# Kernel optimization log

Measured on AMD Instinct MI355X. Metric: run time of the kernel, lower is better.

Reference implementation:

```python
import jax, jax.numpy as jnp
import numpy as np

C, D, K15, K16, OUT = 64, 8, 15, 16, 512
B = 32768


def setup_inputs() -> dict:
    key = jax.random.key(0)
    kx, kS, kH, kT, kL = jax.random.split(key, 5)
    x = jax.random.normal(kx, (B, C * D), dtype=jnp.float32)
    S = jax.random.normal(kS, (C, D, K15), dtype=jnp.float32)
    H = jax.random.normal(kH, (K15, K16), dtype=jnp.float32)
    T = jax.random.normal(kT, (C, K15), dtype=jnp.float32)
    LUT = jax.random.normal(kL, (C, K16, OUT), dtype=jnp.float32)
    return {"x": x, "S": S, "H": H, "T": T, "LUT": LUT}


def reference(x, S, H, T, LUT):
    b = x.shape[0]
    xv = x.reshape(b, C, D)                              # (B, C, D)
    p = jnp.einsum('bcd,cdk->bck', xv, S) - T            # (B, C, 15)
    # torch sets zeros to -1 before sign => sign(x)==-1 when x<=0
    s = jnp.where(p > 0, jnp.float32(1.0), jnp.float32(-1.0))
    h = jnp.einsum('bck,kj->bcj', s, H)                  # (B, C, 16)
    idx = jnp.argmax(h, axis=-1)                         # (B, C) int
    # one_hot @ LUT == direct gather of LUT[c, idx[b,c], :]
    vals = LUT[jnp.arange(C)[None, :], idx]              # (B, C, OUT)
    return jnp.sum(vals, axis=1)                         # (B, OUT)
```

## Files before the change

kernel.cpp:

```cpp
#include <hip/hip_runtime.h>
#include <stdint.h>

#define B_    32768
#define C_    64
#define D_    8
#define K15_  15
#define K16_  16
#define OUT_  512

typedef _Float16 half4v __attribute__((ext_vector_type(4)));
typedef _Float16 half8  __attribute__((ext_vector_type(8)));
typedef uint32_t uint4v __attribute__((ext_vector_type(4)));

#define AMAP_OFF  0
#define AMAP_SZ   32768
#define S64_OFF   32768
#define S64_SZ    (64 * 15 * 8 * 8)
#define T64_OFF   (S64_OFF + S64_SZ)
#define T64_SZ    (64 * 15 * 8)
#define IDX_OFF   (T64_OFF + T64_SZ)
#define IDX_SZ    (B_ * C_)
#define S32_SZ    (64 * 15 * 8 * 4)
#define PCT_OFF   (IDX_OFF + IDX_SZ)
#define PCT_SZ    (B_ * 32)
#define PTAB_OFF  (PCT_OFF + PCT_SZ)
#define PTAB_SZ   (32 * 32 * 256 * 16 * 2)
#define WS_NEED   ((size_t)PTAB_OFF + PTAB_SZ)

__device__ __forceinline__ void gld_lds16(const void* g, void* l) {
    __builtin_amdgcn_global_load_lds(
        (const __attribute__((address_space(1))) void*)g,
        (__attribute__((address_space(3))) void*)l, 16, 0, 0);
}

__device__ __forceinline__ void fma_mix_lo(float& acc, uint32_t w, float one) {
    asm("v_fma_mix_f32 %0, %1, %2, %0 op_sel_hi:[1,0,0]"
        : "+v"(acc) : "v"(w), "v"(one));
}
__device__ __forceinline__ void fma_mix_hi(float& acc, uint32_t w, float one) {
    asm("v_fma_mix_f32 %0, %1, %2, %0 op_sel:[1,0,0] op_sel_hi:[1,0,0]"
        : "+v"(acc) : "v"(w), "v"(one));
}

__global__ __launch_bounds__(256) void k_setup(const float* __restrict__ LUT,
                                               const float* __restrict__ H,
                                               const float* __restrict__ S,
                                               const float* __restrict__ T,
                                               _Float16* __restrict__ P5,
                                               uint8_t* __restrict__ amap,
                                               double* __restrict__ S64,
                                               double* __restrict__ T64,
                                               float* __restrict__ S32,
                                               float* __restrict__ T32,
                                               int do_pairs) {
    int gid = blockIdx.x * 256 + threadIdx.x;

    if (do_pairs) {
        int e8 = gid & 1;
        int q = (gid >> 1) & 255;
        int jc = (gid >> 9) & 31;
        int p = gid >> 14;
        int t0 = q >> 4;
        int t1 = q & 15;
        int j0 = jc * 16 + e8 * 8;
        const float* u = LUT + (size_t)((2 * p) * 16 + t0) * 512 + j0;
        const float* v = LUT + (size_t)((2 * p + 1) * 16 + t1) * 512 + j0;
        float4 u0 = ((const float4*)u)[0];
        float4 u1 = ((const float4*)u)[1];
        float4 v0 = ((const float4*)v)[0];
        float4 v1 = ((const float4*)v)[1];
        half8 w;
        w[0] = (_Float16)(u0.x + v0.x);
        w[1] = (_Float16)(u0.y + v0.y);
        w[2] = (_Float16)(u0.z + v0.z);
        w[3] = (_Float16)(u0.w + v0.w);
        w[4] = (_Float16)(u1.x + v1.x);
        w[5] = (_Float16)(u1.y + v1.y);
        w[6] = (_Float16)(u1.z + v1.z);
        w[7] = (_Float16)(u1.w + v1.w);
        *(half8*)(P5 + (size_t)gid * 8) = w;
    }

    if (blockIdx.x < 128) {
        int code = gid;
        double h[K16_];
#pragma unroll
        for (int j = 0; j < K16_; ++j) h[j] = 0.0;
#pragma unroll
        for (int k = 0; k < K15_; ++k) {
            double s = ((code >> k) & 1) ? 1.0 : -1.0;
#pragma unroll
            for (int j = 0; j < K16_; ++j) h[j] += s * (double)H[k * K16_ + j];
        }
        double best = h[0];
        int bi = 0;
#pragma unroll
        for (int j = 1; j < K16_; ++j) {
            if (h[j] > best) { best = h[j]; bi = j; }
        }
        amap[code] = (uint8_t)bi;
    } else if (blockIdx.x == 128) {
        for (int i = threadIdx.x; i < 64 * 15 * 8; i += 256) {
            int c = i / 120;
            int r = i - c * 120;
            int k = r >> 3;
            int d = r & 7;
            float sv = S[c * 120 + d * 15 + k];
            S64[i] = (double)sv;
            if (do_pairs) S32[i] = sv;
        }
        for (int i = threadIdx.x; i < 64 * 15; i += 256) {
            T64[i] = (double)T[i];
            if (do_pairs) T32[i] = T[i];
        }
    }
}

#define XST3 579
#define CPAD2 24
template <int FAST>
__global__ __launch_bounds__(256, 6) void k_codes5(const float* __restrict__ x,
                                                   const double* __restrict__ S64,
                                                   const double* __restrict__ T64,
                                                   const float* __restrict__ S32,
                                                   const float* __restrict__ T32,
                                                   const uint8_t* __restrict__ amap,
                                                   uint8_t* __restrict__ idxo,
                                                   uint8_t* __restrict__ pcT) {
    __shared__ float xls[8 * XST3];
    __shared__ alignas(16) uint16_t codesh[64 * CPAD2];

    int bg = blockIdx.x >> 2;
    int cq = blockIdx.x & 3;
    int b0 = bg * 64;
    int lane = threadIdx.x & 63;
    int wv = __builtin_amdgcn_readfirstlane(threadIdx.x >> 6);
    int tid = threadIdx.x;

    float4 rgA[4], rgB[4];
#pragma unroll
    for (int t2 = 0; t2 < 4; ++t2) {
        int e = t2 * 256 + tid;
        int b = e >> 4;
        int j4 = e & 15;
        rgA[t2] = *(const float4*)(x + (size_t)(b0 + b) * 512 + cq * 128 +
                                   0 * 64 + j4 * 4);
    }
#pragma unroll
    for (int t2 = 0; t2 < 4; ++t2) {
        int e = t2 * 256 + tid;
        int b = e >> 4;
        int j4 = e & 15;
        int cl = j4 >> 1;
        int d0 = (j4 & 1) * 4;
        float* dst = &xls[cl * XST3 + b * 9 + d0];
        dst[0] = rgA[t2].x; dst[1] = rgA[t2].y;
        dst[2] = rgA[t2].z; dst[3] = rgA[t2].w;
    }
    __syncthreads();

#pragma unroll
    for (int t2 = 0; t2 < 4; ++t2) {
        int e = t2 * 256 + tid;
        int b = e >> 4;
        int j4 = e & 15;
        rgB[t2] = *(const float4*)(x + (size_t)(b0 + b) * 512 + cq * 128 +
                                   1 * 64 + j4 * 4);
    }

#pragma unroll
    for (int r = 0; r < 2; ++r) {
#pragma unroll
        for (int i = 0; i < 2; ++i) {
            int cl = wv + i * 4;
            int c = cq * 16 + r * 8 + cl;
            unsigned code = 0;
            if (FAST) {
                const float* Sc = S32 + c * 120;
                const float* Tc = T32 + c * 15;
                float xf[8];
#pragma unroll
                for (int d = 0; d < 8; ++d)
                    xf[d] = xls[cl * XST3 + lane * 9 + d];
                float pmin = 3.0e38f;
#pragma unroll
                for (int k = 0; k < K15_; ++k) {
                    float p = -Tc[k];
#pragma unroll
                    for (int d = 0; d < 8; ++d)
                        p = fmaf(xf[d], Sc[k * 8 + d], p);
                    code |= (p > 0.f) ? (1u << k) : 0u;
                    pmin = fminf(pmin, fabsf(p));
                }
                if (pmin < 1e-4f) {
                    const double* Sd = S64 + c * 120;
                    const double* Td = T64 + c * 15;
                    code = 0;
#pragma unroll
                    for (int k = 0; k < K15_; ++k) {
                        double p = -Td[k];
#pragma unroll
                        for (int d = 0; d < 8; ++d)
                            p = fma((double)xf[d], Sd[k * 8 + d], p);
                        code |= (p > 0.0) ? (1u << k) : 0u;
                    }
                }
            } else {
                const double* Sc = S64 + c * 120;
                const double* Tc = T64 + c * 15;
                double xd[8];
#pragma unroll
                for (int d = 0; d < 8; ++d)
                    xd[d] = (double)xls[cl * XST3 + lane * 9 + d];
#pragma unroll
                for (int k = 0; k < K15_; ++k) {
                    double p = -Tc[k];
#pragma unroll
                    for (int d = 0; d < 8; ++d)
                        p = fma(xd[d], Sc[k * 8 + d], p);
                    code |= (p > 0.0) ? (1u << k) : 0u;
                }
            }
            codesh[lane * CPAD2 + r * 8 + cl] = (uint16_t)code;
        }
        if (r == 0) {
            __syncthreads();
#pragma unroll
            for (int t2 = 0; t2 < 4; ++t2) {
                int e = t2 * 256 + tid;
                int b = e >> 4;
                int j4 = e & 15;
                int cl = j4 >> 1;
                int d0 = (j4 & 1) * 4;
                float* dst = &xls[cl * XST3 + b * 9 + d0];
                dst[0] = rgB[t2].x; dst[1] = rgB[t2].y;
                dst[2] = rgB[t2].z; dst[3] = rgB[t2].w;
            }
            __syncthreads();
        }
    }
    __syncthreads();

    int bb = tid >> 2;
    int sub = tid & 3;
    uint64_t cw8 = *(const uint64_t*)&codesh[bb * CPAD2 + sub * 4];
    uint16_t cds[4];
    cds[0] = (uint16_t)(cw8 & 0xFFFF);
    cds[1] = (uint16_t)((cw8 >> 16) & 0xFFFF);
    cds[2] = (uint16_t)((cw8 >> 32) & 0xFFFF);
    cds[3] = (uint16_t)(cw8 >> 48);
    uint8_t ids[4];
#pragma unroll
    for (int j = 0; j < 4; ++j) ids[j] = amap[cds[j]];

    if (FAST) {
        int row = b0 + bb;
        int rg = row >> 10;
        int tr = row & 127;
        int i_ = (row & 1023) >> 7;
        uint8_t* base = pcT + rg * 1024 + tr * 8 + i_;
        int p0 = cq * 8 + sub * 2;
        base[(size_t)p0 * 32768] = (uint8_t)((ids[0] << 4) | ids[1]);
        base[(size_t)(p0 + 1) * 32768] = (uint8_t)((ids[2] << 4) | ids[3]);
    } else {
        uint32_t w0 = (uint32_t)ids[0] | ((uint32_t)ids[1] << 8) |
                      ((uint32_t)ids[2] << 16) | ((uint32_t)ids[3] << 24);
        *(uint32_t*)(idxo + (size_t)(b0 + bb) * 64 + cq * 16 + sub * 4) = w0;
    }
}

__global__ __launch_bounds__(256, 8) void k_main9(const uint8_t* __restrict__ pcT,
                                                  const _Float16* __restrict__ P5,
                                                  float* __restrict__ out) {
    __shared__ alignas(16) _Float16 slab[2][256 * 16];

    int rg5 = blockIdx.x >> 5;
    int jc = blockIdx.x & 31;
    int t = threadIdx.x;
    int tc = t & 1;
    int tr = t >> 1;
    int lane = t & 63;
    int wv = __builtin_amdgcn_readfirstlane(t >> 6);

    const uint8_t* cbase = pcT + (rg5 >> 1) * 1024 + tr * 8 + (rg5 & 1) * 4;

    float acc[4][8];
#pragma unroll
    for (int i = 0; i < 4; ++i)
#pragma unroll
        for (int e = 0; e < 8; ++e) acc[i][e] = 0.f;
    float one = 1.0f;

    int hoff = wv * 512 + lane * 8;

    {
        const _Float16* g = P5 + (size_t)jc * 4096 + hoff;
        gld_lds16(g, &slab[0][wv * 512]);
        gld_lds16(g + 2048, &slab[0][wv * 512 + 2048]);
    }
    uint32_t cw = *(const uint32_t*)cbase;
    uint32_t cwn = 0;

    for (int p = 0; p < 32; ++p) {
        __syncthreads();

        if (p < 31) {
            const _Float16* g =
                P5 + (size_t)((p + 1) * 32 + jc) * 4096 + hoff;
            _Float16* d = &slab[(p + 1) & 1][wv * 512];
            gld_lds16(g, d);
            gld_lds16(g + 2048, d + 2048);
            cwn = *(const uint32_t*)(cbase + (size_t)(p + 1) * 32768);
        }

        const _Float16* rb = &slab[p & 1][0] + tc * 8;
        uint32_t cw_cur = cw;
#pragma unroll
        for (int i = 0; i < 4; ++i) {
            int ci = (int)((cw_cur >> (8 * i)) & 0xFF);
            half8 v = *(const half8*)(rb + ci * 16);
            uint4v w = __builtin_bit_cast(uint4v, v);
#pragma unroll
            for (int e2 = 0; e2 < 4; ++e2) {
                fma_mix_lo(acc[i][2 * e2], w[e2], one);
                fma_mix_hi(acc[i][2 * e2 + 1], w[e2], one);
            }
        }
        cw = cwn;
    }

#pragma unroll
    for (int i = 0; i < 4; ++i) {
        int row = rg5 * 512 + i * 128 + tr;
        float* o = out + (size_t)row * 512 + jc * 16 + tc * 8;
        float4 w0;
        w0.x = acc[i][0]; w0.y = acc[i][1]; w0.z = acc[i][2]; w0.w = acc[i][3];
        float4 w1;
        w1.x = acc[i][4]; w1.y = acc[i][5]; w1.z = acc[i][6]; w1.w = acc[i][7];
        ((float4*)o)[0] = w0;
        ((float4*)o)[1] = w1;
    }
}

__global__ __launch_bounds__(256) void k_main_direct(const uint8_t* __restrict__ idx,
                                                     const float* __restrict__ LUT,
                                                     float* __restrict__ out) {
    int j4 = threadIdx.x & 127;
    int sub = threadIdx.x >> 7;
    int b0 = blockIdx.x * 16 + sub * 8;
    const float4* L4 = (const float4*)LUT;
    for (int r = 0; r < 8; ++r) {
        int b = b0 + r;
        const uint32_t* iw = (const uint32_t*)(idx + (size_t)b * 64);
        float4 acc;
        acc.x = 0.f; acc.y = 0.f; acc.z = 0.f; acc.w = 0.f;
#pragma unroll
        for (int i = 0; i < 16; ++i) {
            uint32_t w = __builtin_amdgcn_readfirstlane(iw[i]);
#pragma unroll
            for (int t = 0; t < 4; ++t) {
                int c = i * 4 + t;
                uint32_t codev = (w >> (8 * t)) & 0xFu;
                float4 v = L4[(size_t)(c * 16 + codev) * 128 + j4];
                acc.x += v.x; acc.y += v.y; acc.z += v.z; acc.w += v.w;
            }
        }
        ((float4*)(out + (size_t)b * 512))[j4] = acc;
    }
}

extern "C" void kernel_launch(void* const* d_in, const int* in_sizes, int n_in,
                              void* d_out, int out_size, void* d_ws, size_t ws_size,
                              hipStream_t stream) {
    const float* x   = (const float*)d_in[0];
    const float* S   = (const float*)d_in[1];
    const float* H   = (const float*)d_in[2];
    const float* T   = (const float*)d_in[3];
    const float* LUT = (const float*)d_in[4];
    float* out = (float*)d_out;

    uint8_t* ws = (uint8_t*)d_ws;
    uint8_t* amap = ws + AMAP_OFF;
    double* S64   = (double*)(ws + S64_OFF);
    double* T64   = (double*)(ws + T64_OFF);
    uint8_t* idxb = ws + IDX_OFF;
    float* S32    = (float*)(ws + IDX_OFF);
    float* T32    = (float*)(ws + IDX_OFF + S32_SZ);
    uint8_t* pcTb = ws + PCT_OFF;
    _Float16* P5  = (_Float16*)(ws + PTAB_OFF);

    bool use_pairs = ws_size >= WS_NEED;

    hipLaunchKernelGGL(k_setup, dim3(use_pairs ? 2048 : 129), dim3(256), 0,
                       stream, LUT, H, S, T, P5, amap, S64, T64, S32, T32,
                       use_pairs ? 1 : 0);
    if (use_pairs) {
        hipLaunchKernelGGL((k_codes5<1>), dim3(B_ / 64 * 4), dim3(256), 0,
                           stream, x, S64, T64, S32, T32, amap, idxb, pcTb);
        hipLaunchKernelGGL(k_main9, dim3(2048), dim3(256), 0, stream,
                           pcTb, P5, out);
    } else {
        hipLaunchKernelGGL((k_codes5<0>), dim3(B_ / 64 * 4), dim3(256), 0,
                           stream, x, S64, T64, S32, T32, amap, idxb, pcTb);
        hipLaunchKernelGGL(k_main_direct, dim3(B_ / 16), dim3(256), 0, stream,
                           idxb, LUT, out);
    }
}
```

Baseline: 165.7 us.

## Move pair-table build into codes kernel and triple-buffer main gather loop

```diff
diff --git a/kernel.cpp b/kernel.cpp
--- a/kernel.cpp
+++ b/kernel.cpp
@@ -42,20 +42,70 @@
         : "+v"(acc) : "v"(w), "v"(one));
 }
 
-__global__ __launch_bounds__(256) void k_setup(const float* __restrict__ LUT,
-                                               const float* __restrict__ H,
+__global__ __launch_bounds__(256) void k_setup(const float* __restrict__ H,
                                                const float* __restrict__ S,
                                                const float* __restrict__ T,
-                                               _Float16* __restrict__ P5,
                                                uint8_t* __restrict__ amap,
                                                double* __restrict__ S64,
                                                double* __restrict__ T64,
                                                float* __restrict__ S32,
                                                float* __restrict__ T32,
-                                               int do_pairs) {
+                                               int flags) {
     int gid = blockIdx.x * 256 + threadIdx.x;
 
-    if (do_pairs) {
+    if (blockIdx.x < 128) {
+        int code = gid;
+        double h[K16_];
+#pragma unroll
+        for (int j = 0; j < K16_; ++j) h[j] = 0.0;
+#pragma unroll
+        for (int k = 0; k < K15_; ++k) {
+            double s = ((code >> k) & 1) ? 1.0 : -1.0;
+#pragma unroll
+            for (int j = 0; j < K16_; ++j) h[j] += s * (double)H[k * K16_ + j];
+        }
+        double best = h[0];
+        int bi = 0;
+#pragma unroll
+        for (int j = 1; j < K16_; ++j) {
+            if (h[j] > best) { best = h[j]; bi = j; }
+        }
+        amap[code] = (uint8_t)bi;
+    } else {
+        for (int i = threadIdx.x; i < 64 * 15 * 8; i += 256) {
+            int c = i / 120;
+            int r = i - c * 120;
+            int k = r >> 3;
+            int d = r & 7;
+            float sv = S[c * 120 + d * 15 + k];
+            S64[i] = (double)sv;
+            if (flags & 1) S32[i] = sv;
+        }
+        for (int i = threadIdx.x; i < 64 * 15; i += 256) {
+            T64[i] = (double)T[i];
+            if (flags & 1) T32[i] = T[i];
+        }
+    }
+}
+
+#define XST3 579
+#define CPAD2 24
+template <int FAST>
+__global__ __launch_bounds__(256, 6) void k_codes6(const float* __restrict__ x,
+                                                   const double* __restrict__ S64,
+                                                   const double* __restrict__ T64,
+                                                   const float* __restrict__ S32,
+                                                   const float* __restrict__ T32,
+                                                   const uint8_t* __restrict__ amap,
+                                                   uint8_t* __restrict__ idxo,
+                                                   uint8_t* __restrict__ pcT,
+                                                   const float* __restrict__ LUT,
+                                                   _Float16* __restrict__ P5) {
+    __shared__ float xls[8 * XST3];
+    __shared__ alignas(16) uint16_t codesh[64 * CPAD2];
+
+    if (FAST && blockIdx.x >= 2048) {
+        int gid = (blockIdx.x - 2048) * 256 + threadIdx.x;
         int e8 = gid & 1;
         int q = (gid >> 1) & 255;
         int jc = (gid >> 9) & 31;
@@ -79,56 +129,8 @@
         w[6] = (_Float16)(u1.z + v1.z);
         w[7] = (_Float16)(u1.w + v1.w);
         *(half8*)(P5 + (size_t)gid * 8) = w;
-    }
-
-    if (blockIdx.x < 128) {
-        int code = gid;
-        double h[K16_];
-#pragma unroll
-        for (int j = 0; j < K16_; ++j) h[j] = 0.0;
-#pragma unroll
-        for (int k = 0; k < K15_; ++k) {
-            double s = ((code >> k) & 1) ? 1.0 : -1.0;
-#pragma unroll
-            for (int j = 0; j < K16_; ++j) h[j] += s * (double)H[k * K16_ + j];
-        }
-        double best = h[0];
-        int bi = 0;
-#pragma unroll
-        for (int j = 1; j < K16_; ++j) {
-            if (h[j] > best) { best = h[j]; bi = j; }
-        }
-        amap[code] = (uint8_t)bi;
-    } else if (blockIdx.x == 128) {
-        for (int i = threadIdx.x; i < 64 * 15 * 8; i += 256) {
-            int c = i / 120;
-            int r = i - c * 120;
-            int k = r >> 3;
-            int d = r & 7;
-            float sv = S[c * 120 + d * 15 + k];
-            S64[i] = (double)sv;
-            if (do_pairs) S32[i] = sv;
-        }
-        for (int i = threadIdx.x; i < 64 * 15; i += 256) {
-            T64[i] = (double)T[i];
-            if (do_pairs) T32[i] = T[i];
-        }
-    }
-}
-
-#define XST3 579
-#define CPAD2 24
-template <int FAST>
-__global__ __launch_bounds__(256, 6) void k_codes5(const float* __restrict__ x,
-                                                   const double* __restrict__ S64,
-                                                   const double* __restrict__ T64,
-                                                   const float* __restrict__ S32,
-                                                   const float* __restrict__ T32,
-                                                   const uint8_t* __restrict__ amap,
-                                                   uint8_t* __restrict__ idxo,
-                                                   uint8_t* __restrict__ pcT) {
-    __shared__ float xls[8 * XST3];
-    __shared__ alignas(16) uint16_t codesh[64 * CPAD2];
+        return;
+    }
 
     int bg = blockIdx.x >> 2;
     int cq = blockIdx.x & 3;
@@ -144,32 +146,26 @@
         int b = e >> 4;
         int j4 = e & 15;
         rgA[t2] = *(const float4*)(x + (size_t)(b0 + b) * 512 + cq * 128 +
-                                   0 * 64 + j4 * 4);
-    }
-#pragma unroll
-    for (int t2 = 0; t2 < 4; ++t2) {
-        int e = t2 * 256 + tid;
-        int b = e >> 4;
-        int j4 = e & 15;
-        int cl = j4 >> 1;
-        int d0 = (j4 & 1) * 4;
-        float* dst = &xls[cl * XST3 + b * 9 + d0];
-        dst[0] = rgA[t2].x; dst[1] = rgA[t2].y;
-        dst[2] = rgA[t2].z; dst[3] = rgA[t2].w;
-    }
-    __syncthreads();
-
-#pragma unroll
-    for (int t2 = 0; t2 < 4; ++t2) {
-        int e = t2 * 256 + tid;
-        int b = e >> 4;
-        int j4 = e & 15;
+                                   j4 * 4);
         rgB[t2] = *(const float4*)(x + (size_t)(b0 + b) * 512 + cq * 128 +
-                                   1 * 64 + j4 * 4);
+                                   64 + j4 * 4);
+        asm volatile("" :: "v"(rgB[t2].x));
     }
 
 #pragma unroll
     for (int r = 0; r < 2; ++r) {
+#pragma unroll
+        for (int t2 = 0; t2 < 4; ++t2) {
+            int e = t2 * 256 + tid;
+            int b = e >> 4;
+            int j4 = e & 15;
+            int cl = j4 >> 1;
+            int d0 = (j4 & 1) * 4;
+            float4 v = (r == 0) ? rgA[t2] : rgB[t2];
+            float* dst = &xls[cl * XST3 + b * 9 + d0];
+            dst[0] = v.x; dst[1] = v.y; dst[2] = v.z; dst[3] = v.w;
+        }
+        __syncthreads();
 #pragma unroll
         for (int i = 0; i < 2; ++i) {
             int cl = wv + i * 4;
@@ -223,23 +219,8 @@
             }
             codesh[lane * CPAD2 + r * 8 + cl] = (uint16_t)code;
         }
-        if (r == 0) {
-            __syncthreads();
-#pragma unroll
-            for (int t2 = 0; t2 < 4; ++t2) {
-                int e = t2 * 256 + tid;
-                int b = e >> 4;
-                int j4 = e & 15;
-                int cl = j4 >> 1;
-                int d0 = (j4 & 1) * 4;
-                float* dst = &xls[cl * XST3 + b * 9 + d0];
-                dst[0] = rgB[t2].x; dst[1] = rgB[t2].y;
-                dst[2] = rgB[t2].z; dst[3] = rgB[t2].w;
-            }
-            __syncthreads();
-        }
-    }
-    __syncthreads();
+        __syncthreads();
+    }
 
     int bb = tid >> 2;
     int sub = tid & 3;
@@ -269,10 +250,10 @@
     }
 }
 
-__global__ __launch_bounds__(256, 8) void k_main9(const uint8_t* __restrict__ pcT,
-                                                  const _Float16* __restrict__ P5,
-                                                  float* __restrict__ out) {
-    __shared__ alignas(16) _Float16 slab[2][256 * 16];
+__global__ __launch_bounds__(256, 5) void k_main10(const uint8_t* __restrict__ pcT,
+                                                   const _Float16* __restrict__ P5,
+                                                   float* __restrict__ out) {
+    __shared__ alignas(16) _Float16 slab[3][256 * 16];
 
     int rg5 = blockIdx.x >> 5;
     int jc = blockIdx.x & 31;
@@ -284,6 +265,13 @@
 
     const uint8_t* cbase = pcT + (rg5 >> 1) * 1024 + tr * 8 + (rg5 & 1) * 4;
 
+    uint32_t cw[32];
+#pragma unroll
+    for (int p = 0; p < 32; ++p)
+        cw[p] = *(const uint32_t*)(cbase + (size_t)p * 32768);
+#pragma unroll
+    for (int p = 0; p < 32; ++p) asm volatile("" :: "v"(cw[p]));
+
     float acc[4][8];
 #pragma unroll
     for (int i = 0; i < 4; ++i)
@@ -294,27 +282,32 @@
     int hoff = wv * 512 + lane * 8;
 
     {
-        const _Float16* g = P5 + (size_t)jc * 4096 + hoff;
-        gld_lds16(g, &slab[0][wv * 512]);
-        gld_lds16(g + 2048, &slab[0][wv * 512 + 2048]);
-    }
-    uint32_t cw = *(const uint32_t*)cbase;
-    uint32_t cwn = 0;
-
+        const _Float16* g0 = P5 + (size_t)jc * 4096 + hoff;
+        gld_lds16(g0, &slab[0][wv * 512]);
+        gld_lds16(g0 + 2048, &slab[0][wv * 512 + 2048]);
+        const _Float16* g1 = P5 + (size_t)(32 + jc) * 4096 + hoff;
+        gld_lds16(g1, &slab[1][wv * 512]);
+        gld_lds16(g1 + 2048, &slab[1][wv * 512 + 2048]);
+    }
+
+#pragma unroll
     for (int p = 0; p < 32; ++p) {
-        __syncthreads();
-
-        if (p < 31) {
+        if (p < 31) asm volatile("s_waitcnt vmcnt(2)");
+        else        asm volatile("s_waitcnt vmcnt(0)");
+        __builtin_amdgcn_sched_barrier(0);
+        __builtin_amdgcn_s_barrier();
+        __builtin_amdgcn_sched_barrier(0);
+
+        if (p < 30) {
             const _Float16* g =
-                P5 + (size_t)((p + 1) * 32 + jc) * 4096 + hoff;
-            _Float16* d = &slab[(p + 1) & 1][wv * 512];
+                P5 + (size_t)((p + 2) * 32 + jc) * 4096 + hoff;
+            _Float16* d = &slab[(p + 2) % 3][wv * 512];
             gld_lds16(g, d);
             gld_lds16(g + 2048, d + 2048);
-            cwn = *(const uint32_t*)(cbase + (size_t)(p + 1) * 32768);
-        }
-
-        const _Float16* rb = &slab[p & 1][0] + tc * 8;
-        uint32_t cw_cur = cw;
+        }
+
+        const _Float16* rb = &slab[p % 3][0] + tc * 8;
+        uint32_t cw_cur = cw[p];
 #pragma unroll
         for (int i = 0; i < 4; ++i) {
             int ci = (int)((cw_cur >> (8 * i)) & 0xFF);
@@ -326,7 +319,6 @@
                 fma_mix_hi(acc[i][2 * e2 + 1], w[e2], one);
             }
         }
-        cw = cwn;
     }
 
 #pragma unroll
@@ -391,17 +383,16 @@
 
     bool use_pairs = ws_size >= WS_NEED;
 
-    hipLaunchKernelGGL(k_setup, dim3(use_pairs ? 2048 : 129), dim3(256), 0,
-                       stream, LUT, H, S, T, P5, amap, S64, T64, S32, T32,
-                       use_pairs ? 1 : 0);
+    hipLaunchKernelGGL(k_setup, dim3(129), dim3(256), 0, stream,
+                       H, S, T, amap, S64, T64, S32, T32, use_pairs ? 1 : 0);
     if (use_pairs) {
-        hipLaunchKernelGGL((k_codes5<1>), dim3(B_ / 64 * 4), dim3(256), 0,
-                           stream, x, S64, T64, S32, T32, amap, idxb, pcTb);
-        hipLaunchKernelGGL(k_main9, dim3(2048), dim3(256), 0, stream,
+        hipLaunchKernelGGL((k_codes6<1>), dim3(4096), dim3(256), 0, stream,
+                           x, S64, T64, S32, T32, amap, idxb, pcTb, LUT, P5);
+        hipLaunchKernelGGL(k_main10, dim3(2048), dim3(256), 0, stream,
                            pcTb, P5, out);
     } else {
-        hipLaunchKernelGGL((k_codes5<0>), dim3(B_ / 64 * 4), dim3(256), 0,
-                           stream, x, S64, T64, S32, T32, amap, idxb, pcTb);
+        hipLaunchKernelGGL((k_codes6<0>), dim3(2048), dim3(256), 0, stream,
+                           x, S64, T64, S32, T32, amap, idxb, pcTb, LUT, P5);
         hipLaunchKernelGGL(k_main_direct, dim3(B_ / 16), dim3(256), 0, stream,
                            idxb, LUT, out);
     }
```

New measurement: 167.0 us. About the same (+0.8%).
